# Kernel optimization log

Hardware: AMD Instinct MI355X
Metric: run time of the kernel (lower is better)

Reference implementation:

```python
import jax, jax.numpy as jnp
import numpy as np

N_NODES = 100000
D_IN = 256
D_OUT = 128
N_EDGES = 1600000
KEEP_PROB = 0.5  # tf.nn.dropout(input, 1 - 0.5) -> rate = 0.5


def setup_inputs() -> dict:
    key = jax.random.key(0)
    k_x, k_mask, k_w, k_row, k_col, k_ew = jax.random.split(key, 6)
    x = jax.random.normal(k_x, (N_NODES, D_IN), dtype=jnp.float32)
    # Deterministic scaled dropout keep-mask: Bernoulli(keep)/keep
    u = jax.random.uniform(k_mask, (N_NODES, D_IN), dtype=jnp.float32)
    dropout_mask = (u < KEEP_PROB).astype(jnp.float32) / KEEP_PROB
    kernel = jax.random.normal(k_w, (D_IN, D_OUT), dtype=jnp.float32) * (1.0 / np.sqrt(D_IN))
    edge_row = jax.random.randint(k_row, (N_EDGES,), 0, N_NODES, dtype=jnp.int32)
    edge_col = jax.random.randint(k_col, (N_EDGES,), 0, N_NODES, dtype=jnp.int32)
    edge_weight = jax.random.uniform(k_ew, (N_EDGES,), dtype=jnp.float32)
    return {"x": x, "dropout_mask": dropout_mask, "kernel": kernel,
            "edge_row": edge_row, "edge_col": edge_col, "edge_weight": edge_weight}


def reference(x, dropout_mask, kernel, edge_row, edge_col, edge_weight):
    # dropout (mask already scaled by 1/keep_prob)
    h = x * dropout_mask                      # [N, D_IN]
    # dense projection
    h = h @ kernel                            # [N, D_OUT]
    # sparse (COO) adjacency @ dense: out[r] += w_e * h[c] for each edge (r, c)
    msgs = edge_weight[:, None] * h[edge_col]            # [E, D_OUT]
    agg = jax.ops.segment_sum(msgs, edge_row, num_segments=N_NODES)  # [N, D_OUT]
    # act=True -> relu
    return jax.nn.relu(agg)
```

## Files before the change

### kernel.cpp

```cpp
#include <hip/hip_runtime.h>

constexpr int NN = 100000;
constexpr int DI = 256;
constexpr int DO = 128;
constexpr int NE = 1600000;

constexpr int TILE = 2048;
constexpr int RCAP = 64;

constexpr int NGB = (NN + 63) / 64;
constexpr int NPB = (NE + TILE - 1) / TILE;

typedef __bf16 bf16x8 __attribute__((ext_vector_type(8)));
typedef float  f32x4  __attribute__((ext_vector_type(4)));

__device__ inline unsigned short f2bf(float f) {
    union { float f; unsigned u; } v; v.f = f;
    return (unsigned short)((v.u + 0x7FFF + ((v.u >> 16) & 1)) >> 16);
}
__device__ inline float bf2f(unsigned u16) {
    union { unsigned u; float f; } v; v.u = u16 << 16;
    return v.f;
}

__global__ __launch_bounds__(256)
void wt_kernel(const float* __restrict__ W, unsigned short* __restrict__ Wt) {
    __shared__ float t[32][33];
    const int tx = threadIdx.x & 31, ty = threadIdx.x >> 5;
    const int k0 = (blockIdx.x >> 2) * 32, n0 = (blockIdx.x & 3) * 32;
#pragma unroll
    for (int i = 0; i < 32; i += 8)
        t[ty + i][tx] = W[(size_t)(k0 + ty + i) * DO + n0 + tx];
    __syncthreads();
#pragma unroll
    for (int i = 0; i < 32; i += 8)
        Wt[(size_t)(n0 + ty + i) * DI + k0 + tx] = f2bf(t[tx][ty + i]);
}

__global__ __launch_bounds__(256)
void gemm_part_kernel(const float* __restrict__ x, const float* __restrict__ mask,
                      const unsigned short* __restrict__ Wt,
                      unsigned short* __restrict__ h,
                      const int* __restrict__ erow, const int* __restrict__ ecol,
                      const float* __restrict__ ew, int* __restrict__ rcnt,
                      int2* __restrict__ ecsr) {
    __shared__ unsigned short As[64][72];
    __shared__ unsigned short Bs[128][72];

    const int bid = blockIdx.x;
    const bool is_part = (bid < 2 * NPB) && (bid & 1);

    if (!is_part) {
        const int gb   = (bid < 2 * NPB) ? (bid >> 1) : (bid - NPB);
        const int tid  = threadIdx.x;
        const int lane = tid & 63;
        const int w    = tid >> 6;
        const int m0   = gb * 64;
        const int mw   = w * 16;
        const int l15  = lane & 15;
        const int l4   = lane >> 4;

        f32x4 acc[8];
#pragma unroll
        for (int ct = 0; ct < 8; ++ct) acc[ct] = (f32x4){0.f, 0.f, 0.f, 0.f};

        const int lr = tid >> 4;
        const int lk = (tid & 15) * 4;

        float4 xv[4], mv[4];
        const float4 z4 = make_float4(0.f, 0.f, 0.f, 0.f);

#pragma unroll
        for (int p = 0; p < 4; ++p) {
            const int r = m0 + p * 16 + lr;
            if (r < NN) {
                xv[p] = *(const float4*)(x    + (size_t)r * DI + lk);
                mv[p] = *(const float4*)(mask + (size_t)r * DI + lk);
            } else { xv[p] = z4; mv[p] = z4; }
        }

        for (int kc = 0; kc < DI; kc += 64) {
            __syncthreads();
#pragma unroll
            for (int p = 0; p < 4; ++p) {
                ushort4 pk;
                pk.x = f2bf(xv[p].x * mv[p].x); pk.y = f2bf(xv[p].y * mv[p].y);
                pk.z = f2bf(xv[p].z * mv[p].z); pk.w = f2bf(xv[p].w * mv[p].w);
                *(ushort4*)&As[p * 16 + lr][lk] = pk;
            }
            {
                const int kl = (tid & 7) * 8;
#pragma unroll
                for (int p = 0; p < 4; ++p) {
                    const int n = p * 32 + (tid >> 3);
                    *(uint4*)&Bs[n][kl] =
                        *(const uint4*)(Wt + (size_t)n * DI + kc + kl);
                }
            }
            if (kc + 64 < DI) {
#pragma unroll
                for (int p = 0; p < 4; ++p) {
                    const int r = m0 + p * 16 + lr;
                    if (r < NN) {
                        xv[p] = *(const float4*)(x    + (size_t)r * DI + kc + 64 + lk);
                        mv[p] = *(const float4*)(mask + (size_t)r * DI + kc + 64 + lk);
                    } else { xv[p] = z4; mv[p] = z4; }
                }
            }
            __syncthreads();
#pragma unroll
            for (int ks = 0; ks < 2; ++ks) {
                const int ko = ks * 32 + l4 * 8;
                const bf16x8 a0 = *(const bf16x8*)&As[mw + l15][ko];
#pragma unroll
                for (int ct = 0; ct < 8; ++ct) {
                    const bf16x8 b = *(const bf16x8*)&Bs[ct * 16 + l15][ko];
                    acc[ct] = __builtin_amdgcn_mfma_f32_16x16x32_bf16(a0, b, acc[ct], 0, 0, 0);
                }
            }
        }
#pragma unroll
        for (int ct = 0; ct < 8; ++ct)
#pragma unroll
            for (int reg = 0; reg < 4; ++reg) {
                const int row = m0 + mw + l4 * 4 + reg;
                if (row < NN)
                    h[(size_t)row * DO + ct * 16 + l15] = f2bf(acc[ct][reg]);
            }
    } else {
        const int t  = threadIdx.x;
        const int e0 = (bid >> 1) * TILE;
#pragma unroll 4
        for (int k = 0; k < TILE; k += 256) {
            const int e = e0 + k + t;
            if (e < NE) {
                const int row = erow[e];
                const int pos = atomicAdd(&rcnt[row], 1);
                if (pos < RCAP) {
                    int2 v;
                    v.x = ecol[e];
                    v.y = __float_as_int(ew[e]);
                    ecsr[(size_t)row * RCAP + pos] = v;
                }
            }
        }
    }
}

__device__ inline void acc8(float* acc, const uint4& q, float w) {
    const unsigned* u = (const unsigned*)&q;
#pragma unroll
    for (int i = 0; i < 4; ++i) {
        acc[2 * i + 0] += w * bf2f(u[i] & 0xFFFF);
        acc[2 * i + 1] += w * bf2f(u[i] >> 16);
    }
}

__global__ __launch_bounds__(256)
void bgather_kernel(const unsigned short* __restrict__ h,
                    const int* __restrict__ rcnt,
                    const int2* __restrict__ ecsr, float* __restrict__ out) {
    const int t   = threadIdx.x;
    const int l16 = t & 15, g = t >> 4;
    const int gid0 = blockIdx.x * 16 + g;
    const int ngrp = gridDim.x * 16;
    const int ho   = l16 * 8;

    for (int r = gid0; r < NN; r += ngrp) {
        int deg = rcnt[r];
        if (deg > RCAP) deg = RCAP;
        const int2* ep = ecsr + (size_t)r * RCAP;

        float acc[8];
#pragma unroll
        for (int i = 0; i < 8; ++i) acc[i] = 0.f;

        int j = 0;
        for (; j + 8 <= deg; j += 8) {
            const uint4 d0 = *(const uint4*)(ep + j);
            const uint4 d1 = *(const uint4*)(ep + j + 2);
            const uint4 d2 = *(const uint4*)(ep + j + 4);
            const uint4 d3 = *(const uint4*)(ep + j + 6);
            const uint4 q0 = *(const uint4*)(h + (size_t)d0.x * DO + ho);
            const uint4 q1 = *(const uint4*)(h + (size_t)d0.z * DO + ho);
            const uint4 q2 = *(const uint4*)(h + (size_t)d1.x * DO + ho);
            const uint4 q3 = *(const uint4*)(h + (size_t)d1.z * DO + ho);
            const uint4 q4 = *(const uint4*)(h + (size_t)d2.x * DO + ho);
            const uint4 q5 = *(const uint4*)(h + (size_t)d2.z * DO + ho);
            const uint4 q6 = *(const uint4*)(h + (size_t)d3.x * DO + ho);
            const uint4 q7 = *(const uint4*)(h + (size_t)d3.z * DO + ho);
            acc8(acc, q0, __int_as_float(d0.y));
            acc8(acc, q1, __int_as_float(d0.w));
            acc8(acc, q2, __int_as_float(d1.y));
            acc8(acc, q3, __int_as_float(d1.w));
            acc8(acc, q4, __int_as_float(d2.y));
            acc8(acc, q5, __int_as_float(d2.w));
            acc8(acc, q6, __int_as_float(d3.y));
            acc8(acc, q7, __int_as_float(d3.w));
        }
        for (; j + 2 <= deg; j += 2) {
            const int2 e0 = ep[j], e1 = ep[j + 1];
            const uint4 q0 = *(const uint4*)(h + (size_t)e0.x * DO + ho);
            const uint4 q1 = *(const uint4*)(h + (size_t)e1.x * DO + ho);
            acc8(acc, q0, __int_as_float(e0.y));
            acc8(acc, q1, __int_as_float(e1.y));
        }
        if (j < deg) {
            const int2 e0 = ep[j];
            const uint4 q0 = *(const uint4*)(h + (size_t)e0.x * DO + ho);
            acc8(acc, q0, __int_as_float(e0.y));
        }
        float* op = out + (size_t)r * DO + ho;
        *(float4*)(op + 0) = make_float4(fmaxf(acc[0], 0.f), fmaxf(acc[1], 0.f),
                                         fmaxf(acc[2], 0.f), fmaxf(acc[3], 0.f));
        *(float4*)(op + 4) = make_float4(fmaxf(acc[4], 0.f), fmaxf(acc[5], 0.f),
                                         fmaxf(acc[6], 0.f), fmaxf(acc[7], 0.f));
    }
}

extern "C" void kernel_launch(void* const* d_in, const int* in_sizes, int n_in,
                              void* d_out, int out_size, void* d_ws, size_t ws_size,
                              hipStream_t stream) {
    const float* x    = (const float*)d_in[0];
    const float* mask = (const float*)d_in[1];
    const float* W    = (const float*)d_in[2];
    const int*   erow = (const int*)d_in[3];
    const int*   ecol = (const int*)d_in[4];
    const float* ew   = (const float*)d_in[5];
    float* out = (float*)d_out;

    char* p = (char*)d_ws;
    unsigned short* h  = (unsigned short*)p;  p += (size_t)NN * DO * 2;
    unsigned short* Wt = (unsigned short*)p;  p += (size_t)DO * DI * 2;
    int* rcnt = (int*)p;                      p += (size_t)NN * 4;
    int2* ecsr = (int2*)p;

    hipMemsetAsync(rcnt, 0, (size_t)NN * sizeof(int), stream);

    wt_kernel<<<32, 256, 0, stream>>>(W, Wt);
    gemm_part_kernel<<<NGB + NPB, 256, 0, stream>>>(x, mask, Wt, h,
                                                    erow, ecol, ew, rcnt, ecsr);
    bgather_kernel<<<2048, 256, 0, stream>>>(h, rcnt, ecsr, out);
}
```

Baseline: 367.7 us.

## Fuse all stages into one persistent cooperative kernel with grid syncs

Replaces the memset plus three launches with a single cooperative persistent kernel of 1024 blocks. The kernel zeroes the counters, transposes the weights, grid-syncs, then pulls GEMM and edge-partition units from an atomic work counter, grid-syncs again, and runs the gather. The aim is to remove launch gaps and the separate memset, and to balance work dynamically. The cost is grid-sync overhead, an atomic fetch per unit, and the occupancy limit on a cooperative launch. The old multi-kernel path stays as a fallback if the cooperative launch fails.

```diff
diff --git a/kernel.cpp b/kernel.cpp
--- a/kernel.cpp
+++ b/kernel.cpp
@@ -1,4 +1,7 @@
 #include <hip/hip_runtime.h>
+#include <hip/hip_cooperative_groups.h>
+
+namespace cg = cooperative_groups;
 
 constexpr int NN = 100000;
 constexpr int DI = 256;
@@ -8,8 +11,10 @@
 constexpr int TILE = 2048;
 constexpr int RCAP = 64;
 
-constexpr int NGB = (NN + 63) / 64;
-constexpr int NPB = (NE + TILE - 1) / TILE;
+constexpr int NGB    = (NN + 63) / 64;
+constexpr int NPB    = (NE + TILE - 1) / TILE;
+constexpr int NUNITS = NGB + NPB;
+constexpr int GRID   = 1024;
 
 typedef __bf16 bf16x8 __attribute__((ext_vector_type(8)));
 typedef float  f32x4  __attribute__((ext_vector_type(4)));
@@ -22,131 +27,6 @@
     union { unsigned u; float f; } v; v.u = u16 << 16;
     return v.f;
 }
-
-__global__ __launch_bounds__(256)
-void wt_kernel(const float* __restrict__ W, unsigned short* __restrict__ Wt) {
-    __shared__ float t[32][33];
-    const int tx = threadIdx.x & 31, ty = threadIdx.x >> 5;
-    const int k0 = (blockIdx.x >> 2) * 32, n0 = (blockIdx.x & 3) * 32;
-#pragma unroll
-    for (int i = 0; i < 32; i += 8)
-        t[ty + i][tx] = W[(size_t)(k0 + ty + i) * DO + n0 + tx];
-    __syncthreads();
-#pragma unroll
-    for (int i = 0; i < 32; i += 8)
-        Wt[(size_t)(n0 + ty + i) * DI + k0 + tx] = f2bf(t[tx][ty + i]);
-}
-
-__global__ __launch_bounds__(256)
-void gemm_part_kernel(const float* __restrict__ x, const float* __restrict__ mask,
-                      const unsigned short* __restrict__ Wt,
-                      unsigned short* __restrict__ h,
-                      const int* __restrict__ erow, const int* __restrict__ ecol,
-                      const float* __restrict__ ew, int* __restrict__ rcnt,
-                      int2* __restrict__ ecsr) {
-    __shared__ unsigned short As[64][72];
-    __shared__ unsigned short Bs[128][72];
-
-    const int bid = blockIdx.x;
-    const bool is_part = (bid < 2 * NPB) && (bid & 1);
-
-    if (!is_part) {
-        const int gb   = (bid < 2 * NPB) ? (bid >> 1) : (bid - NPB);
-        const int tid  = threadIdx.x;
-        const int lane = tid & 63;
-        const int w    = tid >> 6;
-        const int m0   = gb * 64;
-        const int mw   = w * 16;
-        const int l15  = lane & 15;
-        const int l4   = lane >> 4;
-
-        f32x4 acc[8];
-#pragma unroll
-        for (int ct = 0; ct < 8; ++ct) acc[ct] = (f32x4){0.f, 0.f, 0.f, 0.f};
-
-        const int lr = tid >> 4;
-        const int lk = (tid & 15) * 4;
-
-        float4 xv[4], mv[4];
-        const float4 z4 = make_float4(0.f, 0.f, 0.f, 0.f);
-
-#pragma unroll
-        for (int p = 0; p < 4; ++p) {
-            const int r = m0 + p * 16 + lr;
-            if (r < NN) {
-                xv[p] = *(const float4*)(x    + (size_t)r * DI + lk);
-                mv[p] = *(const float4*)(mask + (size_t)r * DI + lk);
-            } else { xv[p] = z4; mv[p] = z4; }
-        }
-
-        for (int kc = 0; kc < DI; kc += 64) {
-            __syncthreads();
-#pragma unroll
-            for (int p = 0; p < 4; ++p) {
-                ushort4 pk;
-                pk.x = f2bf(xv[p].x * mv[p].x); pk.y = f2bf(xv[p].y * mv[p].y);
-                pk.z = f2bf(xv[p].z * mv[p].z); pk.w = f2bf(xv[p].w * mv[p].w);
-                *(ushort4*)&As[p * 16 + lr][lk] = pk;
-            }
-            {
-                const int kl = (tid & 7) * 8;
-#pragma unroll
-                for (int p = 0; p < 4; ++p) {
-                    const int n = p * 32 + (tid >> 3);
-                    *(uint4*)&Bs[n][kl] =
-                        *(const uint4*)(Wt + (size_t)n * DI + kc + kl);
-                }
-            }
-            if (kc + 64 < DI) {
-#pragma unroll
-                for (int p = 0; p < 4; ++p) {
-                    const int r = m0 + p * 16 + lr;
-                    if (r < NN) {
-                        xv[p] = *(const float4*)(x    + (size_t)r * DI + kc + 64 + lk);
-                        mv[p] = *(const float4*)(mask + (size_t)r * DI + kc + 64 + lk);
-                    } else { xv[p] = z4; mv[p] = z4; }
-                }
-            }
-            __syncthreads();
-#pragma unroll
-            for (int ks = 0; ks < 2; ++ks) {
-                const int ko = ks * 32 + l4 * 8;
-                const bf16x8 a0 = *(const bf16x8*)&As[mw + l15][ko];
-#pragma unroll
-                for (int ct = 0; ct < 8; ++ct) {
-                    const bf16x8 b = *(const bf16x8*)&Bs[ct * 16 + l15][ko];
-                    acc[ct] = __builtin_amdgcn_mfma_f32_16x16x32_bf16(a0, b, acc[ct], 0, 0, 0);
-                }
-            }
-        }
-#pragma unroll
-        for (int ct = 0; ct < 8; ++ct)
-#pragma unroll
-            for (int reg = 0; reg < 4; ++reg) {
-                const int row = m0 + mw + l4 * 4 + reg;
-                if (row < NN)
-                    h[(size_t)row * DO + ct * 16 + l15] = f2bf(acc[ct][reg]);
-            }
-    } else {
-        const int t  = threadIdx.x;
-        const int e0 = (bid >> 1) * TILE;
-#pragma unroll 4
-        for (int k = 0; k < TILE; k += 256) {
-            const int e = e0 + k + t;
-            if (e < NE) {
-                const int row = erow[e];
-                const int pos = atomicAdd(&rcnt[row], 1);
-                if (pos < RCAP) {
-                    int2 v;
-                    v.x = ecol[e];
-                    v.y = __float_as_int(ew[e]);
-                    ecsr[(size_t)row * RCAP + pos] = v;
-                }
-            }
-        }
-    }
-}
-
 __device__ inline void acc8(float* acc, const uint4& q, float w) {
     const unsigned* u = (const unsigned*)&q;
 #pragma unroll
@@ -156,17 +36,145 @@
     }
 }
 
-__global__ __launch_bounds__(256)
-void bgather_kernel(const unsigned short* __restrict__ h,
-                    const int* __restrict__ rcnt,
-                    const int2* __restrict__ ecsr, float* __restrict__ out) {
-    const int t   = threadIdx.x;
-    const int l16 = t & 15, g = t >> 4;
-    const int gid0 = blockIdx.x * 16 + g;
-    const int ngrp = gridDim.x * 16;
-    const int ho   = l16 * 8;
-
-    for (int r = gid0; r < NN; r += ngrp) {
+__global__ __launch_bounds__(256, 4)
+void mega_kernel(const float* __restrict__ x, const float* __restrict__ mask,
+                 const float* __restrict__ W, unsigned short* __restrict__ Wt,
+                 unsigned short* __restrict__ h,
+                 const int* __restrict__ erow, const int* __restrict__ ecol,
+                 const float* __restrict__ ew, int* __restrict__ rcnt,
+                 int2* __restrict__ ecsr, float* __restrict__ out,
+                 int* __restrict__ wctr) {
+    __shared__ union SMu {
+        float t[32][33];
+        struct { unsigned short As[64][72]; unsigned short Bs[128][72]; } g;
+    } sm;
+    __shared__ int s_u;
+
+    const int tid = threadIdx.x;
+    const int bid = blockIdx.x;
+
+    for (int i = bid * 256 + tid; i < NN; i += GRID * 256) rcnt[i] = 0;
+    if (bid == 0 && tid == 0) *wctr = 0;
+    if (bid < 32) {
+        const int tx = tid & 31, ty = tid >> 5;
+        const int k0 = (bid >> 2) * 32, n0 = (bid & 3) * 32;
+#pragma unroll
+        for (int i = 0; i < 32; i += 8)
+            sm.t[ty + i][tx] = W[(size_t)(k0 + ty + i) * DO + n0 + tx];
+        __syncthreads();
+#pragma unroll
+        for (int i = 0; i < 32; i += 8)
+            Wt[(size_t)(n0 + ty + i) * DI + k0 + tx] = f2bf(sm.t[tx][ty + i]);
+    }
+    cg::this_grid().sync();
+
+    for (;;) {
+        if (tid == 0) s_u = atomicAdd(wctr, 1);
+        __syncthreads();
+        const int u = s_u;
+        if (u >= NUNITS) break;
+        const bool is_part = (u < 2 * NPB) && (u & 1);
+
+        if (!is_part) {
+            const int gb   = (u < 2 * NPB) ? (u >> 1) : (u - NPB);
+            const int lane = tid & 63;
+            const int w    = tid >> 6;
+            const int m0   = gb * 64;
+            const int mw   = w * 16;
+            const int l15  = lane & 15;
+            const int l4   = lane >> 4;
+
+            f32x4 acc[8];
+#pragma unroll
+            for (int ct = 0; ct < 8; ++ct) acc[ct] = (f32x4){0.f, 0.f, 0.f, 0.f};
+
+            const int lr = tid >> 4;
+            const int lk = (tid & 15) * 4;
+
+            float4 xv[4], mv[4];
+            const float4 z4 = make_float4(0.f, 0.f, 0.f, 0.f);
+
+#pragma unroll
+            for (int p = 0; p < 4; ++p) {
+                const int r = m0 + p * 16 + lr;
+                if (r < NN) {
+                    xv[p] = *(const float4*)(x    + (size_t)r * DI + lk);
+                    mv[p] = *(const float4*)(mask + (size_t)r * DI + lk);
+                } else { xv[p] = z4; mv[p] = z4; }
+            }
+
+            for (int kc = 0; kc < DI; kc += 64) {
+                __syncthreads();
+#pragma unroll
+                for (int p = 0; p < 4; ++p) {
+                    ushort4 pk;
+                    pk.x = f2bf(xv[p].x * mv[p].x); pk.y = f2bf(xv[p].y * mv[p].y);
+                    pk.z = f2bf(xv[p].z * mv[p].z); pk.w = f2bf(xv[p].w * mv[p].w);
+                    *(ushort4*)&sm.g.As[p * 16 + lr][lk] = pk;
+                }
+                {
+                    const int kl = (tid & 7) * 8;
+#pragma unroll
+                    for (int p = 0; p < 4; ++p) {
+                        const int n = p * 32 + (tid >> 3);
+                        *(uint4*)&sm.g.Bs[n][kl] =
+                            *(const uint4*)(Wt + (size_t)n * DI + kc + kl);
+                    }
+                }
+                if (kc + 64 < DI) {
+#pragma unroll
+                    for (int p = 0; p < 4; ++p) {
+                        const int r = m0 + p * 16 + lr;
+                        if (r < NN) {
+                            xv[p] = *(const float4*)(x    + (size_t)r * DI + kc + 64 + lk);
+                            mv[p] = *(const float4*)(mask + (size_t)r * DI + kc + 64 + lk);
+                        } else { xv[p] = z4; mv[p] = z4; }
+                    }
+                }
+                __syncthreads();
+#pragma unroll
+                for (int ks = 0; ks < 2; ++ks) {
+                    const int ko = ks * 32 + l4 * 8;
+                    const bf16x8 a0 = *(const bf16x8*)&sm.g.As[mw + l15][ko];
+#pragma unroll
+                    for (int ct = 0; ct < 8; ++ct) {
+                        const bf16x8 b = *(const bf16x8*)&sm.g.Bs[ct * 16 + l15][ko];
+                        acc[ct] = __builtin_amdgcn_mfma_f32_16x16x32_bf16(a0, b, acc[ct], 0, 0, 0);
+                    }
+                }
+            }
+#pragma unroll
+            for (int ct = 0; ct < 8; ++ct)
+#pragma unroll
+                for (int reg = 0; reg < 4; ++reg) {
+                    const int row = m0 + mw + l4 * 4 + reg;
+                    if (row < NN)
+                        h[(size_t)row * DO + ct * 16 + l15] = f2bf(acc[ct][reg]);
+                }
+        } else {
+            const int e0 = (u >> 1) * TILE;
+#pragma unroll 4
+            for (int k = 0; k < TILE; k += 256) {
+                const int e = e0 + k + tid;
+                if (e < NE) {
+                    const int row = erow[e];
+                    const int pos = atomicAdd(&rcnt[row], 1);
+                    if (pos < RCAP) {
+                        int2 v;
+                        v.x = ecol[e];
+                        v.y = __float_as_int(ew[e]);
+                        ecsr[(size_t)row * RCAP + pos] = v;
+                    }
+                }
+            }
+        }
+        __syncthreads();
+    }
+    cg::this_grid().sync();
+
+    const int l16 = tid & 15, g = tid >> 4;
+    const int ho  = l16 * 8;
+    for (int r = bid * 16 + g; r < NN; r += GRID * 16) {
         int deg = rcnt[r];
         if (deg > RCAP) deg = RCAP;
         const int2* ep = ecsr + (size_t)r * RCAP;
@@ -218,6 +226,192 @@
     }
 }
 
+__global__ __launch_bounds__(256)
+void wt_kernel(const float* __restrict__ W, unsigned short* __restrict__ Wt) {
+    __shared__ float t[32][33];
+    const int tx = threadIdx.x & 31, ty = threadIdx.x >> 5;
+    const int k0 = (blockIdx.x >> 2) * 32, n0 = (blockIdx.x & 3) * 32;
+#pragma unroll
+    for (int i = 0; i < 32; i += 8)
+        t[ty + i][tx] = W[(size_t)(k0 + ty + i) * DO + n0 + tx];
+    __syncthreads();
+#pragma unroll
+    for (int i = 0; i < 32; i += 8)
+        Wt[(size_t)(n0 + ty + i) * DI + k0 + tx] = f2bf(t[tx][ty + i]);
+}
+
+__global__ __launch_bounds__(256)
+void gemm_part_kernel(const float* __restrict__ x, const float* __restrict__ mask,
+                      const unsigned short* __restrict__ Wt,
+                      unsigned short* __restrict__ h,
+                      const int* __restrict__ erow, const int* __restrict__ ecol,
+                      const float* __restrict__ ew, int* __restrict__ rcnt,
+                      int2* __restrict__ ecsr) {
+    __shared__ unsigned short As[64][72];
+    __shared__ unsigned short Bs[128][72];
+
+    const int bid = blockIdx.x;
+    const bool is_part = (bid < 2 * NPB) && (bid & 1);
+
+    if (!is_part) {
+        const int gb   = (bid < 2 * NPB) ? (bid >> 1) : (bid - NPB);
+        const int tid  = threadIdx.x;
+        const int lane = tid & 63;
+        const int w    = tid >> 6;
+        const int m0   = gb * 64;
+        const int mw   = w * 16;
+        const int l15  = lane & 15;
+        const int l4   = lane >> 4;
+
+        f32x4 acc[8];
+#pragma unroll
+        for (int ct = 0; ct < 8; ++ct) acc[ct] = (f32x4){0.f, 0.f, 0.f, 0.f};
+
+        const int lr = tid >> 4;
+        const int lk = (tid & 15) * 4;
+
+        float4 xv[4], mv[4];
+        const float4 z4 = make_float4(0.f, 0.f, 0.f, 0.f);
+
+#pragma unroll
+        for (int p = 0; p < 4; ++p) {
+            const int r = m0 + p * 16 + lr;
+            if (r < NN) {
+                xv[p] = *(const float4*)(x    + (size_t)r * DI + lk);
+                mv[p] = *(const float4*)(mask + (size_t)r * DI + lk);
+            } else { xv[p] = z4; mv[p] = z4; }
+        }
+
+        for (int kc = 0; kc < DI; kc += 64) {
+            __syncthreads();
+#pragma unroll
+            for (int p = 0; p < 4; ++p) {
+                ushort4 pk;
+                pk.x = f2bf(xv[p].x * mv[p].x); pk.y = f2bf(xv[p].y * mv[p].y);
+                pk.z = f2bf(xv[p].z * mv[p].z); pk.w = f2bf(xv[p].w * mv[p].w);
+                *(ushort4*)&As[p * 16 + lr][lk] = pk;
+            }
+            {
+                const int kl = (tid & 7) * 8;
+#pragma unroll
+                for (int p = 0; p < 4; ++p) {
+                    const int n = p * 32 + (tid >> 3);
+                    *(uint4*)&Bs[n][kl] =
+                        *(const uint4*)(Wt + (size_t)n * DI + kc + kl);
+                }
+            }
+            if (kc + 64 < DI) {
+#pragma unroll
+                for (int p = 0; p < 4; ++p) {
+                    const int r = m0 + p * 16 + lr;
+                    if (r < NN) {
+                        xv[p] = *(const float4*)(x    + (size_t)r * DI + kc + 64 + lk);
+                        mv[p] = *(const float4*)(mask + (size_t)r * DI + kc + 64 + lk);
+                    } else { xv[p] = z4; mv[p] = z4; }
+                }
+            }
+            __syncthreads();
+#pragma unroll
+            for (int ks = 0; ks < 2; ++ks) {
+                const int ko = ks * 32 + l4 * 8;
+                const bf16x8 a0 = *(const bf16x8*)&As[mw + l15][ko];
+#pragma unroll
+                for (int ct = 0; ct < 8; ++ct) {
+                    const bf16x8 b = *(const bf16x8*)&Bs[ct * 16 + l15][ko];
+                    acc[ct] = __builtin_amdgcn_mfma_f32_16x16x32_bf16(a0, b, acc[ct], 0, 0, 0);
+                }
+            }
+        }
+#pragma unroll
+        for (int ct = 0; ct < 8; ++ct)
+#pragma unroll
+            for (int reg = 0; reg < 4; ++reg) {
+                const int row = m0 + mw + l4 * 4 + reg;
+                if (row < NN)
+                    h[(size_t)row * DO + ct * 16 + l15] = f2bf(acc[ct][reg]);
+            }
+    } else {
+        const int t  = threadIdx.x;
+        const int e0 = (bid >> 1) * TILE;
+#pragma unroll 4
+        for (int k = 0; k < TILE; k += 256) {
+            const int e = e0 + k + t;
+            if (e < NE) {
+                const int row = erow[e];
+                const int pos = atomicAdd(&rcnt[row], 1);
+                if (pos < RCAP) {
+                    int2 v;
+                    v.x = ecol[e];
+                    v.y = __float_as_int(ew[e]);
+                    ecsr[(size_t)row * RCAP + pos] = v;
+                }
+            }
+        }
+    }
+}
+
+__global__ __launch_bounds__(256)
+void bgather_kernel(const unsigned short* __restrict__ h,
+                    const int* __restrict__ rcnt,
+                    const int2* __restrict__ ecsr, float* __restrict__ out) {
+    const int t   = threadIdx.x;
+    const int l16 = t & 15, g = t >> 4;
+    const int gid0 = blockIdx.x * 16 + g;
+    const int ngrp = gridDim.x * 16;
+    const int ho   = l16 * 8;
+
+    for (int r = gid0; r < NN; r += ngrp) {
+        int deg = rcnt[r];
+        if (deg > RCAP) deg = RCAP;
+        const int2* ep = ecsr + (size_t)r * RCAP;
+
+        float acc[8];
+#pragma unroll
+        for (int i = 0; i < 8; ++i) acc[i] = 0.f;
+
+        int j = 0;
+        for (; j + 8 <= deg; j += 8) {
+            const uint4 d0 = *(const uint4*)(ep + j);
+            const uint4 d1 = *(const uint4*)(ep + j + 2);
+            const uint4 d2 = *(const uint4*)(ep + j + 4);
+            const uint4 d3 = *(const uint4*)(ep + j + 6);
+            const uint4 q0 = *(const uint4*)(h + (size_t)d0.x * DO + ho);
+            const uint4 q1 = *(const uint4*)(h + (size_t)d0.z * DO + ho);
+            const uint4 q2 = *(const uint4*)(h + (size_t)d1.x * DO + ho);
+            const uint4 q3 = *(const uint4*)(h + (size_t)d1.z * DO + ho);
+            const uint4 q4 = *(const uint4*)(h + (size_t)d2.x * DO + ho);
+            const uint4 q5 = *(const uint4*)(h + (size_t)d2.z * DO + ho);
+            const uint4 q6 = *(const uint4*)(h + (size_t)d3.x * DO + ho);
+            const uint4 q7 = *(const uint4*)(h + (size_t)d3.z * DO + ho);
+            acc8(acc, q0, __int_as_float(d0.y));
+            acc8(acc, q1, __int_as_float(d0.w));
+            acc8(acc, q2, __int_as_float(d1.y));
+            acc8(acc, q3, __int_as_float(d1.w));
+            acc8(acc, q4, __int_as_float(d2.y));
+            acc8(acc, q5, __int_as_float(d2.w));
+            acc8(acc, q6, __int_as_float(d3.y));
+            acc8(acc, q7, __int_as_float(d3.w));
+        }
+        for (; j + 2 <= deg; j += 2) {
+            const int2 e0 = ep[j], e1 = ep[j + 1];
+            const uint4 q0 = *(const uint4*)(h + (size_t)e0.x * DO + ho);
+            const uint4 q1 = *(const uint4*)(h + (size_t)e1.x * DO + ho);
+            acc8(acc, q0, __int_as_float(e0.y));
+            acc8(acc, q1, __int_as_float(e1.y));
+        }
+        if (j < deg) {
+            const int2 e0 = ep[j];
+            const uint4 q0 = *(const uint4*)(h + (size_t)e0.x * DO + ho);
+            acc8(acc, q0, __int_as_float(e0.y));
+        }
+        float* op = out + (size_t)r * DO + ho;
+        *(float4*)(op + 0) = make_float4(fmaxf(acc[0], 0.f), fmaxf(acc[1], 0.f),
+                                         fmaxf(acc[2], 0.f), fmaxf(acc[3], 0.f));
+        *(float4*)(op + 4) = make_float4(fmaxf(acc[4], 0.f), fmaxf(acc[5], 0.f),
+                                         fmaxf(acc[6], 0.f), fmaxf(acc[7], 0.f));
+    }
+}
+
 extern "C" void kernel_launch(void* const* d_in, const int* in_sizes, int n_in,
                               void* d_out, int out_size, void* d_ws, size_t ws_size,
                               hipStream_t stream) {
@@ -233,12 +427,20 @@
     unsigned short* h  = (unsigned short*)p;  p += (size_t)NN * DO * 2;
     unsigned short* Wt = (unsigned short*)p;  p += (size_t)DO * DI * 2;
     int* rcnt = (int*)p;                      p += (size_t)NN * 4;
+    int* wctr = (int*)p;                      p += 256;
     int2* ecsr = (int2*)p;
 
-    hipMemsetAsync(rcnt, 0, (size_t)NN * sizeof(int), stream);
-
-    wt_kernel<<<32, 256, 0, stream>>>(W, Wt);
-    gemm_part_kernel<<<NGB + NPB, 256, 0, stream>>>(x, mask, Wt, h,
-                                                    erow, ecol, ew, rcnt, ecsr);
-    bgather_kernel<<<2048, 256, 0, stream>>>(h, rcnt, ecsr, out);
-}
+    void* args[] = {(void*)&x, (void*)&mask, (void*)&W, (void*)&Wt, (void*)&h,
+                    (void*)&erow, (void*)&ecol, (void*)&ew, (void*)&rcnt,
+                    (void*)&ecsr, (void*)&out, (void*)&wctr};
+    hipError_t err = hipLaunchCooperativeKernel((const void*)mega_kernel,
+                                                dim3(GRID), dim3(256),
+                                                args, 0, stream);
+    if (err != hipSuccess) {
+        hipMemsetAsync(rcnt, 0, (size_t)NN * sizeof(int), stream);
+        wt_kernel<<<32, 256, 0, stream>>>(W, Wt);
+        gemm_part_kernel<<<NGB + NPB, 256, 0, stream>>>(x, mask, Wt, h,
+                                                        erow, ecol, ew, rcnt, ecsr);
+        bgather_kernel<<<2048, 256, 0, stream>>>(h, rcnt, ecsr, out);
+    }
+}
```

After: 601.9 us. 1.64x slower.
